# Kernel tuning notes

Measured on AMD Instinct MI355X. Metric: run time of the kernel, lower is better.

## Reference

```python
import jax, jax.numpy as jnp
import numpy as np

D_MODEL = 1024
N_HEAD = 16
D_HEAD = D_MODEL // N_HEAD


def setup_inputs() -> dict:
    key = jax.random.key(0)
    k1, k2, k3 = jax.random.split(key, 3)
    x = jax.random.normal(k1, (4, 1024, D_MODEL), dtype=jnp.float32)
    # torch Linear(d_model, 3*d_model, bias=False): weight [3*d_model, d_model], y = x @ W.T
    w_qkv = jax.random.normal(k2, (3 * D_MODEL, D_MODEL), dtype=jnp.float32) * (1.0 / np.sqrt(D_MODEL))
    w_out = jax.random.normal(k3, (D_MODEL, D_MODEL), dtype=jnp.float32) * (1.0 / np.sqrt(D_MODEL))
    return {"x": x, "w_qkv": w_qkv, "w_out": w_out}


def reference(x, w_qkv, w_out):
    B, T, C = x.shape
    qkv = x @ w_qkv.T                                   # [B,T,3C]
    qkv = qkv.reshape(B, T, 3, N_HEAD, D_HEAD)
    q = jnp.transpose(qkv[:, :, 0], (0, 2, 1, 3))       # [B,H,T,Dh]
    k = jnp.transpose(qkv[:, :, 1], (0, 2, 1, 3))
    v = jnp.transpose(qkv[:, :, 2], (0, 2, 1, 3))
    att = jnp.einsum('bhqd,bhkd->bhqk', q, k) / jnp.sqrt(jnp.float32(D_HEAD))
    causal = jnp.tril(jnp.ones((T, T), dtype=bool))
    att = jnp.where(causal[None, None], att, -jnp.inf)
    att = jax.nn.softmax(att, axis=-1)
    y = jnp.einsum('bhqk,bhkd->bhqd', att, v)           # [B,H,T,Dh]
    y = jnp.transpose(y, (0, 2, 1, 3)).reshape(B, T, C)
    return y @ w_out.T
```

## Files before the change

kernel.cpp:

```cpp
#include <hip/hip_runtime.h>
#include <hip/hip_bf16.h>
#include <stdint.h>

#define DM 1024
#define NH 16
#define DH 64
#define BB 4
#define TT 1024
#define MR (BB*TT)

typedef __attribute__((ext_vector_type(8))) short bf16x8;
typedef __attribute__((ext_vector_type(4))) float f32x4;

typedef unsigned int __attribute__((address_space(1))) uint_g;
typedef unsigned int __attribute__((address_space(3))) uint_l;

static __device__ __forceinline__ void gload_lds16(const void* g, void* l) {
  __builtin_amdgcn_global_load_lds((const uint_g*)g, (uint_l*)l, 16, 0, 0);
}

static __device__ __forceinline__ unsigned short f2bf(float f) {
  union { float f; unsigned int u; } v; v.f = f;
  unsigned int r = v.u + 0x7fffu + ((v.u >> 16) & 1u);
  return (unsigned short)(r >> 16);
}
static __device__ __forceinline__ unsigned short f2bf_fast(float f) {
  union { float f; unsigned int u; } v; v.f = f;
  return (unsigned short)((v.u + 0x8000u) >> 16);
}

__global__ __launch_bounds__(256) void k_cvt3(const float* __restrict__ x,
    const float* __restrict__ w1, const float* __restrict__ w2,
    unsigned short* __restrict__ xb, unsigned short* __restrict__ wqb,
    unsigned short* __restrict__ wob) {
  const int n1 = (MR * DM) / 4, n2 = (3 * DM * DM) / 4, n3 = (DM * DM) / 4;
  const int total = n1 + n2 + n3;
  for (int u = blockIdx.x * 256 + threadIdx.x; u < total; u += gridDim.x * 256) {
    const float* src; unsigned short* dst; int i;
    if (u < n1)           { src = x;  dst = xb;  i = u; }
    else if (u < n1 + n2) { src = w1; dst = wqb; i = u - n1; }
    else                  { src = w2; dst = wob; i = u - n1 - n2; }
    float4 v = reinterpret_cast<const float4*>(src)[i];
    ushort4 o;
    o.x = f2bf(v.x); o.y = f2bf(v.y); o.z = f2bf(v.z); o.w = f2bf(v.w);
    reinterpret_cast<ushort4*>(dst)[i] = o;
  }
}

template<int EPI>
__global__ __launch_bounds__(256) void k_gemm(
    const unsigned short* __restrict__ A, const unsigned short* __restrict__ Bw,
    float* __restrict__ Of, unsigned short* __restrict__ qb,
    unsigned short* __restrict__ kb, unsigned short* __restrict__ vtb,
    int N, int K, int tiles_n) {
  __shared__ unsigned short At[2][128 * 32];
  __shared__ unsigned short Bt[2][128 * 32];
  int tid = threadIdx.x;
  int w = tid >> 6, l = tid & 63;
  int l15 = l & 15, k8 = l >> 4;
  int nwg = gridDim.x;
  int cpx = nwg >> 3;
  int wg = blockIdx.x;
  int swz = (wg & 7) * cpx + (wg >> 3);
  int tm = swz / tiles_n, tn = swz % tiles_n;
  int m0 = tm << 7, n0 = tn << 7;

  f32x4 acc[4][4];
  #pragma unroll
  for (int i = 0; i < 4; ++i)
    #pragma unroll
    for (int j = 0; j < 4; ++j) acc[i][j] = (f32x4){0.f, 0.f, 0.f, 0.f};

  int srow = (w << 4) + (l >> 2);
  int sch = l & 3;
  int mrb = ((w >> 1) << 6) + l15;
  int nrb = ((w & 1) << 6) + l15;

  auto stage = [&](int buf, int kk) {
    #pragma unroll
    for (int p = 0; p < 2; ++p) {
      int row = srow + (p << 6);
      int c = sch ^ ((row >> 1) & 3);
      int seg = w + (p << 2);
      gload_lds16(A + (size_t)(m0 + row) * K + kk + (c << 3), &At[buf][seg << 9]);
      gload_lds16(Bw + (size_t)(n0 + row) * K + kk + (c << 3), &Bt[buf][seg << 9]);
    }
  };

  stage(0, 0);
  __syncthreads();
  int cur = 0;
  for (int kk = 0; kk < K; kk += 32) {
    if (kk + 32 < K) stage(cur ^ 1, kk + 32);
    bf16x8 a[4], b[4];
    #pragma unroll
    for (int mf = 0; mf < 4; ++mf) {
      int row = mrb + (mf << 4);
      a[mf] = *(const bf16x8*)&At[cur][(row << 5) + ((k8 ^ ((row >> 1) & 3)) << 3)];
    }
    #pragma unroll
    for (int nf = 0; nf < 4; ++nf) {
      int row = nrb + (nf << 4);
      b[nf] = *(const bf16x8*)&Bt[cur][(row << 5) + ((k8 ^ ((row >> 1) & 3)) << 3)];
    }
    #pragma unroll
    for (int mf = 0; mf < 4; ++mf)
      #pragma unroll
      for (int nf = 0; nf < 4; ++nf)
        acc[mf][nf] = __builtin_amdgcn_mfma_f32_16x16x32_bf16(a[mf], b[nf], acc[mf][nf], 0, 0, 0);
    __syncthreads();
    cur ^= 1;
  }

  #pragma unroll
  for (int mf = 0; mf < 4; ++mf) {
    #pragma unroll
    for (int nf = 0; nf < 4; ++nf) {
      int n = n0 + ((w & 1) << 6) + (nf << 4) + l15;
      int m_base = m0 + ((w >> 1) << 6) + (mf << 4) + (k8 << 2);
      if (EPI == 1) {
        #pragma unroll
        for (int r = 0; r < 4; ++r)
          Of[(size_t)(m_base + r) * N + n] = acc[mf][nf][r];
      } else {
        int s = n >> 10, rem = n & 1023;
        int h = rem >> 6, d = rem & 63;
        #pragma unroll
        for (int r = 0; r < 4; ++r) {
          int m = m_base + r;
          int bb = m >> 10, t = m & 1023;
          float v = acc[mf][nf][r];
          if (s == 0)
            qb[((size_t)(bb * NH + h) * TT + t) * DH + d] = f2bf(v * 0.125f);
          else if (s == 1)
            kb[((size_t)(bb * NH + h) * TT + t) * DH + d] = f2bf(v);
          else
            vtb[((size_t)(bb * NH + h) * DH + d) * TT + t] = f2bf(v);
        }
      }
    }
  }
}

__global__ __launch_bounds__(512) void k_attn(
    const unsigned short* __restrict__ qb, const unsigned short* __restrict__ kb,
    const unsigned short* __restrict__ vtb, unsigned short* __restrict__ yb) {
  __shared__ unsigned short Kt[2][64 * 64];
  __shared__ unsigned short Vt[2][64 * 64];
  __shared__ unsigned short Pl[8][16][72];
  int tid = threadIdx.x, w = tid >> 6, l = tid & 63;
  int l15 = l & 15, k8 = l >> 4;
  int bh = blockIdx.x >> 3;
  int qt = blockIdx.x & 7;
  int q0 = qt << 7;
  const unsigned short* Kb = kb + (size_t)bh * TT * DH;
  const unsigned short* Vb = vtb + (size_t)bh * DH * TT;
  const unsigned short* Qb = qb + (size_t)bh * TT * DH;

  int qrow = q0 + (w << 4) + l15;
  bf16x8 qf[2];
  #pragma unroll
  for (int c = 0; c < 2; ++c)
    qf[c] = *(const bf16x8*)&Qb[(size_t)qrow * DH + (c << 5) + (k8 << 3)];

  f32x4 y[4];
  #pragma unroll
  for (int i = 0; i < 4; ++i) y[i] = (f32x4){0.f, 0.f, 0.f, 0.f};
  float mrow = -INFINITY, lrow = 0.f;

  int srow = l >> 3;
  int sch = l & 7;

  auto stage = [&](int buf, int j0) {
    int row = (w << 3) + srow;
    int c = sch ^ (row & 7);
    gload_lds16(Kb + (size_t)(j0 + row) * DH + (c << 3), &Kt[buf][(w << 3) << 6]);
    gload_lds16(Vb + (size_t)row * TT + j0 + (c << 3), &Vt[buf][(w << 3) << 6]);
  };

  stage(0, 0);
  __syncthreads();
  int cur = 0;

  for (int j0 = 0; j0 < q0 + 128; j0 += 64) {
    if (j0 + 64 < q0 + 128) stage(cur ^ 1, j0 + 64);

    f32x4 s[4];
    #pragma unroll
    for (int f = 0; f < 4; ++f) s[f] = (f32x4){0.f, 0.f, 0.f, 0.f};
    #pragma unroll
    for (int c = 0; c < 2; ++c) {
      #pragma unroll
      for (int f = 0; f < 4; ++f) {
        int row = (f << 4) + l15;
        bf16x8 ak = *(const bf16x8*)&Kt[cur][(row << 6) + ((((c << 2) + k8) ^ (row & 7)) << 3)];
        s[f] = __builtin_amdgcn_mfma_f32_16x16x32_bf16(ak, qf[c], s[f], 0, 0, 0);
      }
    }

    if (j0 + 64 > q0 + (w << 4)) {
      #pragma unroll
      for (int f = 0; f < 4; ++f)
        #pragma unroll
        for (int r = 0; r < 4; ++r)
          if (j0 + (f << 4) + (k8 << 2) + r > qrow) s[f][r] = -INFINITY;
    }

    float pmax = -INFINITY;
    #pragma unroll
    for (int f = 0; f < 4; ++f)
      #pragma unroll
      for (int r = 0; r < 4; ++r) pmax = fmaxf(pmax, s[f][r]);
    pmax = fmaxf(pmax, __shfl_xor(pmax, 16, 64));
    pmax = fmaxf(pmax, __shfl_xor(pmax, 32, 64));

    bool skip = __all(pmax - mrow <= 8.0f);
    float mnew = skip ? mrow : fmaxf(mrow, pmax);
    float psum = 0.f;
    #pragma unroll
    for (int f = 0; f < 4; ++f)
      #pragma unroll
      for (int r = 0; r < 4; ++r) {
        float p = __expf(s[f][r] - mnew);
        s[f][r] = p;
        psum += p;
      }
    psum += __shfl_xor(psum, 16, 64);
    psum += __shfl_xor(psum, 32, 64);
    if (!skip) {
      float alpha = __expf(mrow - mnew);
      lrow *= alpha;
      #pragma unroll
      for (int mf = 0; mf < 4; ++mf) y[mf] *= alpha;
      mrow = mnew;
    }
    lrow += psum;

    #pragma unroll
    for (int f = 0; f < 4; ++f) {
      ushort4 pk;
      pk.x = f2bf_fast(s[f][0]); pk.y = f2bf_fast(s[f][1]);
      pk.z = f2bf_fast(s[f][2]); pk.w = f2bf_fast(s[f][3]);
      *(ushort4*)&Pl[w][l15][(f << 4) + (k8 << 2)] = pk;
    }
    asm volatile("s_waitcnt lgkmcnt(0)" ::: "memory");
    __builtin_amdgcn_sched_barrier(0);

    #pragma unroll
    for (int c = 0; c < 2; ++c) {
      bf16x8 bp = *(const bf16x8*)&Pl[w][l15][(c << 5) + (k8 << 3)];
      #pragma unroll
      for (int mf = 0; mf < 4; ++mf) {
        int dr = (mf << 4) + l15;
        bf16x8 av = *(const bf16x8*)&Vt[cur][(dr << 6) + ((((c << 2) + k8) ^ (dr & 7)) << 3)];
        y[mf] = __builtin_amdgcn_mfma_f32_16x16x32_bf16(av, bp, y[mf], 0, 0, 0);
      }
    }

    __syncthreads();
    cur ^= 1;
  }

  float inv = 1.f / lrow;
  int bb = bh >> 4, h = bh & 15;
  #pragma unroll
  for (int mf = 0; mf < 4; ++mf) {
    ushort4 o;
    o.x = f2bf(y[mf][0] * inv);
    o.y = f2bf(y[mf][1] * inv);
    o.z = f2bf(y[mf][2] * inv);
    o.w = f2bf(y[mf][3] * inv);
    *(ushort4*)&yb[((size_t)(bb * TT + qrow) << 10) + (h << 6) + (mf << 4) + (k8 << 2)] = o;
  }
}

extern "C" void kernel_launch(void* const* d_in, const int* in_sizes, int n_in,
                              void* d_out, int out_size, void* d_ws, size_t ws_size,
                              hipStream_t stream) {
  const float* x    = (const float*)d_in[0];
  const float* wqkv = (const float*)d_in[1];
  const float* wout = (const float*)d_in[2];
  char* ws = (char*)d_ws;
  unsigned short* xb  = (unsigned short*)(ws + (size_t)0);
  unsigned short* wqb = (unsigned short*)(ws + ((size_t)8  << 20));
  unsigned short* wob = (unsigned short*)(ws + ((size_t)14 << 20));
  unsigned short* qbv = (unsigned short*)(ws + ((size_t)16 << 20));
  unsigned short* kbv = (unsigned short*)(ws + ((size_t)24 << 20));
  unsigned short* vtb = (unsigned short*)(ws + ((size_t)32 << 20));
  unsigned short* yb  = (unsigned short*)(ws + ((size_t)40 << 20));

  k_cvt3<<<2048, 256, 0, stream>>>(x, wqkv, wout, xb, wqb, wob);
  k_gemm<0><<<768, 256, 0, stream>>>(xb, wqb, nullptr, qbv, kbv, vtb, 3 * DM, DM, 24);
  k_attn<<<512, 512, 0, stream>>>(qbv, kbv, vtb, yb);
  k_gemm<1><<<256, 256, 0, stream>>>(yb, wob, (float*)d_out, nullptr, nullptr, nullptr, DM, DM, 8);
}
```

Measured before the change: 110.3 us.

## Triple-buffer LDS staging in GEMM and attention with partial vmcnt waits

Both the GEMM and attention kernels move from double to triple LDS buffering, so loads run two tiles ahead. The full __syncthreads is replaced by s_waitcnt vmcnt(N) plus a raw s_barrier, so each iteration waits only for the oldest outstanding tile. The attention kernel also raises wave priority around its MFMA blocks. The cost is more LDS per block, which may reduce occupancy, and the hand-counted vmcnt values must match the number of loads issued.

```diff
diff --git a/kernel.cpp b/kernel.cpp
--- a/kernel.cpp
+++ b/kernel.cpp
@@ -18,6 +18,8 @@
 static __device__ __forceinline__ void gload_lds16(const void* g, void* l) {
   __builtin_amdgcn_global_load_lds((const uint_g*)g, (uint_l*)l, 16, 0, 0);
 }
+
+static __device__ __forceinline__ void fence() { asm volatile("" ::: "memory"); }
 
 static __device__ __forceinline__ unsigned short f2bf(float f) {
   union { float f; unsigned int u; } v; v.f = f;
@@ -53,8 +55,8 @@
     float* __restrict__ Of, unsigned short* __restrict__ qb,
     unsigned short* __restrict__ kb, unsigned short* __restrict__ vtb,
     int N, int K, int tiles_n) {
-  __shared__ unsigned short At[2][128 * 32];
-  __shared__ unsigned short Bt[2][128 * 32];
+  __shared__ unsigned short At[3][128 * 32];
+  __shared__ unsigned short Bt[3][128 * 32];
   int tid = threadIdx.x;
   int w = tid >> 6, l = tid & 63;
   int l15 = l & 15, k8 = l >> 4;
@@ -87,29 +89,36 @@
     }
   };
 
+  const int nt = K >> 5;
   stage(0, 0);
-  __syncthreads();
-  int cur = 0;
-  for (int kk = 0; kk < K; kk += 32) {
-    if (kk + 32 < K) stage(cur ^ 1, kk + 32);
+  stage(1, 32);
+  asm volatile("s_waitcnt vmcnt(4)" ::: "memory");
+  fence(); __builtin_amdgcn_s_barrier(); fence();
+
+  int rd = 0;
+  for (int t = 0; t < nt; ++t) {
+    int st = (rd == 0) ? 2 : rd - 1;
+    if (t + 2 < nt) stage(st, (t + 2) << 5);
     bf16x8 a[4], b[4];
     #pragma unroll
     for (int mf = 0; mf < 4; ++mf) {
       int row = mrb + (mf << 4);
-      a[mf] = *(const bf16x8*)&At[cur][(row << 5) + ((k8 ^ ((row >> 1) & 3)) << 3)];
+      a[mf] = *(const bf16x8*)&At[rd][(row << 5) + ((k8 ^ ((row >> 1) & 3)) << 3)];
     }
     #pragma unroll
     for (int nf = 0; nf < 4; ++nf) {
       int row = nrb + (nf << 4);
-      b[nf] = *(const bf16x8*)&Bt[cur][(row << 5) + ((k8 ^ ((row >> 1) & 3)) << 3)];
+      b[nf] = *(const bf16x8*)&Bt[rd][(row << 5) + ((k8 ^ ((row >> 1) & 3)) << 3)];
     }
     #pragma unroll
     for (int mf = 0; mf < 4; ++mf)
       #pragma unroll
       for (int nf = 0; nf < 4; ++nf)
         acc[mf][nf] = __builtin_amdgcn_mfma_f32_16x16x32_bf16(a[mf], b[nf], acc[mf][nf], 0, 0, 0);
-    __syncthreads();
-    cur ^= 1;
+    if (t + 2 < nt)      { asm volatile("s_waitcnt vmcnt(4)" ::: "memory"); }
+    else if (t + 1 < nt) { asm volatile("s_waitcnt vmcnt(0)" ::: "memory"); }
+    fence(); __builtin_amdgcn_s_barrier(); fence();
+    rd = (rd == 2) ? 0 : rd + 1;
   }
 
   #pragma unroll
@@ -145,8 +154,8 @@
 __global__ __launch_bounds__(512) void k_attn(
     const unsigned short* __restrict__ qb, const unsigned short* __restrict__ kb,
     const unsigned short* __restrict__ vtb, unsigned short* __restrict__ yb) {
-  __shared__ unsigned short Kt[2][64 * 64];
-  __shared__ unsigned short Vt[2][64 * 64];
+  __shared__ unsigned short Kt[3][64 * 64];
+  __shared__ unsigned short Vt[3][64 * 64];
   __shared__ unsigned short Pl[8][16][72];
   int tid = threadIdx.x, w = tid >> 6, l = tid & 63;
   int l15 = l & 15, k8 = l >> 4;
@@ -178,25 +187,32 @@
     gload_lds16(Vb + (size_t)row * TT + j0 + (c << 3), &Vt[buf][(w << 3) << 6]);
   };
 
+  const int ns = (q0 >> 6) + 2;
   stage(0, 0);
-  __syncthreads();
-  int cur = 0;
-
-  for (int j0 = 0; j0 < q0 + 128; j0 += 64) {
-    if (j0 + 64 < q0 + 128) stage(cur ^ 1, j0 + 64);
+  stage(1, 64);
+  asm volatile("s_waitcnt vmcnt(2)" ::: "memory");
+  fence(); __builtin_amdgcn_s_barrier(); fence();
+
+  int rd = 0;
+  for (int t = 0; t < ns; ++t) {
+    int j0 = t << 6;
+    int st = (rd == 0) ? 2 : rd - 1;
+    if (t + 2 < ns) stage(st, (t + 2) << 6);
 
     f32x4 s[4];
     #pragma unroll
     for (int f = 0; f < 4; ++f) s[f] = (f32x4){0.f, 0.f, 0.f, 0.f};
+    __builtin_amdgcn_s_setprio(1);
     #pragma unroll
     for (int c = 0; c < 2; ++c) {
       #pragma unroll
       for (int f = 0; f < 4; ++f) {
         int row = (f << 4) + l15;
-        bf16x8 ak = *(const bf16x8*)&Kt[cur][(row << 6) + ((((c << 2) + k8) ^ (row & 7)) << 3)];
+        bf16x8 ak = *(const bf16x8*)&Kt[rd][(row << 6) + ((((c << 2) + k8) ^ (row & 7)) << 3)];
         s[f] = __builtin_amdgcn_mfma_f32_16x16x32_bf16(ak, qf[c], s[f], 0, 0, 0);
       }
     }
+    __builtin_amdgcn_s_setprio(0);
 
     if (j0 + 64 > q0 + (w << 4)) {
       #pragma unroll
@@ -246,19 +262,23 @@
     asm volatile("s_waitcnt lgkmcnt(0)" ::: "memory");
     __builtin_amdgcn_sched_barrier(0);
 
+    __builtin_amdgcn_s_setprio(1);
     #pragma unroll
     for (int c = 0; c < 2; ++c) {
       bf16x8 bp = *(const bf16x8*)&Pl[w][l15][(c << 5) + (k8 << 3)];
       #pragma unroll
       for (int mf = 0; mf < 4; ++mf) {
         int dr = (mf << 4) + l15;
-        bf16x8 av = *(const bf16x8*)&Vt[cur][(dr << 6) + ((((c << 2) + k8) ^ (dr & 7)) << 3)];
+        bf16x8 av = *(const bf16x8*)&Vt[rd][(dr << 6) + ((((c << 2) + k8) ^ (dr & 7)) << 3)];
         y[mf] = __builtin_amdgcn_mfma_f32_16x16x32_bf16(av, bp, y[mf], 0, 0, 0);
       }
     }
-
-    __syncthreads();
-    cur ^= 1;
+    __builtin_amdgcn_s_setprio(0);
+
+    if (t + 2 < ns)      { asm volatile("s_waitcnt vmcnt(2)" ::: "memory"); }
+    else if (t + 1 < ns) { asm volatile("s_waitcnt vmcnt(0)" ::: "memory"); }
+    fence(); __builtin_amdgcn_s_barrier(); fence();
+    rd = (rd == 2) ? 0 : rd + 1;
   }
 
   float inv = 1.f / lrow;
```

Result: slower. 112.6 us (+2.1%).
